# Optimization experiments

Hardware: AMD Instinct MI355X
Metric: run time of the kernel (lower is better)

Reference implementation:

```python
import jax, jax.numpy as jnp
import numpy as np


def _skew(w):
    # standard hat operator: skew(w) @ u = w x u (matches pytorch3d `hat`)
    x, y, z = w[..., 0], w[..., 1], w[..., 2]
    o = jnp.zeros_like(x)
    return jnp.stack([
        jnp.stack([o, -z, y], -1),
        jnp.stack([z, o, -x], -1),
        jnp.stack([-y, x, o], -1),
    ], -2)


def _se3_exp(dof):
    # pytorch3d se3_exp_map convention: dof[..., :3] = translation log, dof[..., 3:] = rotation log.
    # Returns R (column-vector rotation) and T such that p' = R p + T, equivalent to
    # pytorch3d's row-vector matrix M = [[R^T, 0], [T, 1]] used by Rotate/Translate.
    EPS = 1e-4
    v, w = dof[..., :3], dof[..., 3:]
    theta2 = jnp.sum(w * w, axis=-1)
    theta = jnp.sqrt(theta2)
    small = theta < EPS
    safe_t = jnp.where(small, 1.0, theta)
    safe_t2 = jnp.where(small, 1.0, theta2)
    safe_t3 = jnp.where(small, 1.0, theta2 * theta)
    A = jnp.where(small, 1.0 - theta2 / 6.0, jnp.sin(theta) / safe_t)            # sin(t)/t
    B = jnp.where(small, 0.5 - theta2 / 24.0, (1.0 - jnp.cos(theta)) / safe_t2)  # (1-cos t)/t^2
    C = jnp.where(small, 1.0 / 6.0 - theta2 / 120.0,
                  (theta - jnp.sin(theta)) / safe_t3)                            # (t-sin t)/t^3
    K = _skew(w)
    K2 = K @ K
    I = jnp.eye(3, dtype=dof.dtype)
    R = I + A[..., None, None] * K + B[..., None, None] * K2   # Rodrigues
    V = I + B[..., None, None] * K + C[..., None, None] * K2   # SE3 V-matrix
    T = jnp.einsum('...ij,...j->...i', V, v)
    return R, T


def setup_inputs() -> dict:
    key = jax.random.key(0)
    k1, k2 = jax.random.split(key)
    B, NT, NP = 32, 32, 8192  # batch, teeth, points per tooth
    X_v = jax.random.normal(k1, (B, NT, NP, 3), dtype=jnp.float32)
    dof = jax.random.normal(k2, (B, NT, 6), dtype=jnp.float32)
    return {"X_v": X_v, "dof": dof}


def reference(X_v, dof):
    # Fused, fully batched version of the per-(batch, tooth) loop:
    # assembled[:, t] = Rotate(R[:, t]).compose(Translate(T[:, t])).transform_points(X_v[:, t])
    R, T = _se3_exp(dof)                                   # R: [B,NT,3,3], T: [B,NT,3]
    # row-vector convention p @ R_stored + T with R_stored = R^T  ==  R p + T
    return jnp.einsum('btij,btnj->btni', R, X_v) + T[:, :, None, :]
```

## Files before the change

kernel.cpp:

```cpp
#include <hip/hip_runtime.h>


__global__ __launch_bounds__(256) void se3_apply_kernel(
    const float* __restrict__ X,
    const float* __restrict__ dof,
    float* __restrict__ out,
    int bps)
{
    const int bt  = blockIdx.x / bps;
    const int sub = blockIdx.x % bps;

    const float* d = dof + bt * 6;
    const float vx = d[0], vy = d[1], vz = d[2];
    const float wx = d[3], wy = d[4], wz = d[5];

    const float th2 = wx*wx + wy*wy + wz*wz;
    const float th  = sqrtf(th2);
    float A, Bc, C;
    if (th < 1e-4f) {
        A  = 1.0f - th2 * (1.0f/6.0f);
        Bc = 0.5f - th2 * (1.0f/24.0f);
        C  = (1.0f/6.0f) - th2 * (1.0f/120.0f);
    } else {
        const float s = sinf(th);
        const float c = cosf(th);
        A  = s / th;
        Bc = (1.0f - c) / th2;
        C  = (th - s) / (th2 * th);
    }

    const float r00 = 1.0f + Bc*(wx*wx - th2);
    const float r01 = Bc*wx*wy - A*wz;
    const float r02 = Bc*wx*wz + A*wy;
    const float r10 = Bc*wy*wx + A*wz;
    const float r11 = 1.0f + Bc*(wy*wy - th2);
    const float r12 = Bc*wy*wz - A*wx;
    const float r20 = Bc*wz*wx - A*wy;
    const float r21 = Bc*wz*wy + A*wx;
    const float r22 = 1.0f + Bc*(wz*wz - th2);

    const float q00 = 1.0f + C*(wx*wx - th2);
    const float q01 = C*wx*wy - Bc*wz;
    const float q02 = C*wx*wz + Bc*wy;
    const float q10 = C*wy*wx + Bc*wz;
    const float q11 = 1.0f + C*(wy*wy - th2);
    const float q12 = C*wy*wz - Bc*wx;
    const float q20 = C*wz*wx - Bc*wy;
    const float q21 = C*wz*wy + Bc*wx;
    const float q22 = 1.0f + C*(wz*wz - th2);

    const float Tx = q00*vx + q01*vy + q02*vz;
    const float Ty = q10*vx + q11*vy + q12*vz;
    const float Tz = q20*vx + q21*vy + q22*vz;

    const int base = bt * (bps * 256 * 12) + sub * (256 * 12) + (int)threadIdx.x * 12;
    const float4* Xi = reinterpret_cast<const float4*>(X + base);
    float4*       Oi = reinterpret_cast<float4*>(out + base);

    const float4 a = Xi[0];
    const float4 b = Xi[1];
    const float4 c = Xi[2];

    float o[12];
    {
        const float x = a.x, y = a.y, z = a.z;
        o[0] = fmaf(r00,x, fmaf(r01,y, fmaf(r02,z, Tx)));
        o[1] = fmaf(r10,x, fmaf(r11,y, fmaf(r12,z, Ty)));
        o[2] = fmaf(r20,x, fmaf(r21,y, fmaf(r22,z, Tz)));
    }
    {
        const float x = a.w, y = b.x, z = b.y;
        o[3] = fmaf(r00,x, fmaf(r01,y, fmaf(r02,z, Tx)));
        o[4] = fmaf(r10,x, fmaf(r11,y, fmaf(r12,z, Ty)));
        o[5] = fmaf(r20,x, fmaf(r21,y, fmaf(r22,z, Tz)));
    }
    {
        const float x = b.z, y = b.w, z = c.x;
        o[6] = fmaf(r00,x, fmaf(r01,y, fmaf(r02,z, Tx)));
        o[7] = fmaf(r10,x, fmaf(r11,y, fmaf(r12,z, Ty)));
        o[8] = fmaf(r20,x, fmaf(r21,y, fmaf(r22,z, Tz)));
    }
    {
        const float x = c.y, y = c.z, z = c.w;
        o[9]  = fmaf(r00,x, fmaf(r01,y, fmaf(r02,z, Tx)));
        o[10] = fmaf(r10,x, fmaf(r11,y, fmaf(r12,z, Ty)));
        o[11] = fmaf(r20,x, fmaf(r21,y, fmaf(r22,z, Tz)));
    }

    Oi[0] = make_float4(o[0], o[1], o[2],  o[3]);
    Oi[1] = make_float4(o[4], o[5], o[6],  o[7]);
    Oi[2] = make_float4(o[8], o[9], o[10], o[11]);
}

extern "C" void kernel_launch(void* const* d_in, const int* in_sizes, int n_in,
                              void* d_out, int out_size, void* d_ws, size_t ws_size,
                              hipStream_t stream) {
    const float* X   = (const float*)d_in[0];
    const float* dof = (const float*)d_in[1];
    float* out = (float*)d_out;

    const int BT = in_sizes[1] / 6;
    const int NP = in_sizes[0] / (BT * 3);
    const int bps = (NP * 3) / (256 * 12);

    se3_apply_kernel<<<dim3(BT * bps), dim3(256), 0, stream>>>(X, dof, out, bps);
}
```

Measured before the change: 37.53 us.

## Stage point tiles through LDS for coalesced loads and nontemporal stores

Each thread now loads and stores contiguous float4 strides across the block, so every wavefront access is fully coalesced, and uses shared memory to transpose back to per-thread groups of four points. The SE3 exponential is computed once per block by thread 0 and shared through LDS instead of by every thread. Output is written with nontemporal stores to avoid polluting the cache. The cost is two block barriers and extra LDS traffic per element.

```diff
diff --git a/kernel.cpp b/kernel.cpp
--- a/kernel.cpp
+++ b/kernel.cpp
@@ -1,95 +1,118 @@
 #include <hip/hip_runtime.h>
 
 
-__global__ __launch_bounds__(256) void se3_apply_kernel(
-    const float* __restrict__ X,
+typedef float f4 __attribute__((ext_vector_type(4)));
+
+#define TPB 256
+
+__global__ __launch_bounds__(TPB) void se3_apply_kernel(
+    const f4* __restrict__ X4,
     const float* __restrict__ dof,
-    float* __restrict__ out,
+    f4* __restrict__ O4,
     int bps)
 {
+    __shared__ f4 lds4[768];
+    __shared__ float rt[12];
+
     const int bt  = blockIdx.x / bps;
     const int sub = blockIdx.x % bps;
+    const int t   = (int)threadIdx.x;
 
-    const float* d = dof + bt * 6;
-    const float vx = d[0], vy = d[1], vz = d[2];
-    const float wx = d[3], wy = d[4], wz = d[5];
+    const int base4 = (bt * bps + sub) * 768;
 
-    const float th2 = wx*wx + wy*wy + wz*wz;
-    const float th  = sqrtf(th2);
-    float A, Bc, C;
-    if (th < 1e-4f) {
-        A  = 1.0f - th2 * (1.0f/6.0f);
-        Bc = 0.5f - th2 * (1.0f/24.0f);
-        C  = (1.0f/6.0f) - th2 * (1.0f/120.0f);
-    } else {
-        const float s = sinf(th);
-        const float c = cosf(th);
-        A  = s / th;
-        Bc = (1.0f - c) / th2;
-        C  = (th - s) / (th2 * th);
+    const f4 g0 = X4[base4 + t];
+    const f4 g1 = X4[base4 + 256 + t];
+    const f4 g2 = X4[base4 + 512 + t];
+
+    if (t == 0) {
+        const float* d = dof + bt * 6;
+        const float vx = d[0], vy = d[1], vz = d[2];
+        const float wx = d[3], wy = d[4], wz = d[5];
+        const float th2 = wx*wx + wy*wy + wz*wz;
+        const float th  = sqrtf(th2);
+        float A, Bc, C;
+        if (th < 1e-4f) {
+            A  = 1.0f - th2 * (1.0f/6.0f);
+            Bc = 0.5f - th2 * (1.0f/24.0f);
+            C  = (1.0f/6.0f) - th2 * (1.0f/120.0f);
+        } else {
+            const float s = sinf(th);
+            const float c = cosf(th);
+            A  = s / th;
+            Bc = (1.0f - c) / th2;
+            C  = (th - s) / (th2 * th);
+        }
+        rt[0] = 1.0f + Bc*(wx*wx - th2);
+        rt[1] = Bc*wx*wy - A*wz;
+        rt[2] = Bc*wx*wz + A*wy;
+        rt[3] = Bc*wy*wx + A*wz;
+        rt[4] = 1.0f + Bc*(wy*wy - th2);
+        rt[5] = Bc*wy*wz - A*wx;
+        rt[6] = Bc*wz*wx - A*wy;
+        rt[7] = Bc*wz*wy + A*wx;
+        rt[8] = 1.0f + Bc*(wz*wz - th2);
+        const float q00 = 1.0f + C*(wx*wx - th2);
+        const float q01 = C*wx*wy - Bc*wz;
+        const float q02 = C*wx*wz + Bc*wy;
+        const float q10 = C*wy*wx + Bc*wz;
+        const float q11 = 1.0f + C*(wy*wy - th2);
+        const float q12 = C*wy*wz - Bc*wx;
+        const float q20 = C*wz*wx - Bc*wy;
+        const float q21 = C*wz*wy + Bc*wx;
+        const float q22 = 1.0f + C*(wz*wz - th2);
+        rt[9]  = q00*vx + q01*vy + q02*vz;
+        rt[10] = q10*vx + q11*vy + q12*vz;
+        rt[11] = q20*vx + q21*vy + q22*vz;
     }
 
-    const float r00 = 1.0f + Bc*(wx*wx - th2);
-    const float r01 = Bc*wx*wy - A*wz;
-    const float r02 = Bc*wx*wz + A*wy;
-    const float r10 = Bc*wy*wx + A*wz;
-    const float r11 = 1.0f + Bc*(wy*wy - th2);
-    const float r12 = Bc*wy*wz - A*wx;
-    const float r20 = Bc*wz*wx - A*wy;
-    const float r21 = Bc*wz*wy + A*wx;
-    const float r22 = 1.0f + Bc*(wz*wz - th2);
+    lds4[t]       = g0;
+    lds4[t + 256] = g1;
+    lds4[t + 512] = g2;
+    __syncthreads();
 
-    const float q00 = 1.0f + C*(wx*wx - th2);
-    const float q01 = C*wx*wy - Bc*wz;
-    const float q02 = C*wx*wz + Bc*wy;
-    const float q10 = C*wy*wx + Bc*wz;
-    const float q11 = 1.0f + C*(wy*wy - th2);
-    const float q12 = C*wy*wz - Bc*wx;
-    const float q20 = C*wz*wx - Bc*wy;
-    const float q21 = C*wz*wy + Bc*wx;
-    const float q22 = 1.0f + C*(wz*wz - th2);
+    const float r00 = rt[0], r01 = rt[1], r02 = rt[2];
+    const float r10 = rt[3], r11 = rt[4], r12 = rt[5];
+    const float r20 = rt[6], r21 = rt[7], r22 = rt[8];
+    const float Tx  = rt[9], Ty = rt[10], Tz = rt[11];
 
-    const float Tx = q00*vx + q01*vy + q02*vz;
-    const float Ty = q10*vx + q11*vy + q12*vz;
-    const float Tz = q20*vx + q21*vy + q22*vz;
+    const f4 a = lds4[3*t];
+    const f4 b = lds4[3*t + 1];
+    const f4 c = lds4[3*t + 2];
 
-    const int base = bt * (bps * 256 * 12) + sub * (256 * 12) + (int)threadIdx.x * 12;
-    const float4* Xi = reinterpret_cast<const float4*>(X + base);
-    float4*       Oi = reinterpret_cast<float4*>(out + base);
-
-    const float4 a = Xi[0];
-    const float4 b = Xi[1];
-    const float4 c = Xi[2];
-
-    float o[12];
+    f4 oa, ob, oc;
     {
         const float x = a.x, y = a.y, z = a.z;
-        o[0] = fmaf(r00,x, fmaf(r01,y, fmaf(r02,z, Tx)));
-        o[1] = fmaf(r10,x, fmaf(r11,y, fmaf(r12,z, Ty)));
-        o[2] = fmaf(r20,x, fmaf(r21,y, fmaf(r22,z, Tz)));
+        oa.x = fmaf(r00,x, fmaf(r01,y, fmaf(r02,z, Tx)));
+        oa.y = fmaf(r10,x, fmaf(r11,y, fmaf(r12,z, Ty)));
+        oa.z = fmaf(r20,x, fmaf(r21,y, fmaf(r22,z, Tz)));
     }
     {
         const float x = a.w, y = b.x, z = b.y;
-        o[3] = fmaf(r00,x, fmaf(r01,y, fmaf(r02,z, Tx)));
-        o[4] = fmaf(r10,x, fmaf(r11,y, fmaf(r12,z, Ty)));
-        o[5] = fmaf(r20,x, fmaf(r21,y, fmaf(r22,z, Tz)));
+        oa.w = fmaf(r00,x, fmaf(r01,y, fmaf(r02,z, Tx)));
+        ob.x = fmaf(r10,x, fmaf(r11,y, fmaf(r12,z, Ty)));
+        ob.y = fmaf(r20,x, fmaf(r21,y, fmaf(r22,z, Tz)));
     }
     {
         const float x = b.z, y = b.w, z = c.x;
-        o[6] = fmaf(r00,x, fmaf(r01,y, fmaf(r02,z, Tx)));
-        o[7] = fmaf(r10,x, fmaf(r11,y, fmaf(r12,z, Ty)));
-        o[8] = fmaf(r20,x, fmaf(r21,y, fmaf(r22,z, Tz)));
+        ob.z = fmaf(r00,x, fmaf(r01,y, fmaf(r02,z, Tx)));
+        ob.w = fmaf(r10,x, fmaf(r11,y, fmaf(r12,z, Ty)));
+        oc.x = fmaf(r20,x, fmaf(r21,y, fmaf(r22,z, Tz)));
     }
     {
         const float x = c.y, y = c.z, z = c.w;
-        o[9]  = fmaf(r00,x, fmaf(r01,y, fmaf(r02,z, Tx)));
-        o[10] = fmaf(r10,x, fmaf(r11,y, fmaf(r12,z, Ty)));
-        o[11] = fmaf(r20,x, fmaf(r21,y, fmaf(r22,z, Tz)));
+        oc.y = fmaf(r00,x, fmaf(r01,y, fmaf(r02,z, Tx)));
+        oc.z = fmaf(r10,x, fmaf(r11,y, fmaf(r12,z, Ty)));
+        oc.w = fmaf(r20,x, fmaf(r21,y, fmaf(r22,z, Tz)));
     }
 
-    Oi[0] = make_float4(o[0], o[1], o[2],  o[3]);
-    Oi[1] = make_float4(o[4], o[5], o[6],  o[7]);
-    Oi[2] = make_float4(o[8], o[9], o[10], o[11]);
+    lds4[3*t]     = oa;
+    lds4[3*t + 1] = ob;
+    lds4[3*t + 2] = oc;
+    __syncthreads();
+
+    __builtin_nontemporal_store(lds4[t],       &O4[base4 + t]);
+    __builtin_nontemporal_store(lds4[t + 256], &O4[base4 + 256 + t]);
+    __builtin_nontemporal_store(lds4[t + 512], &O4[base4 + 512 + t]);
 }
 
 extern "C" void kernel_launch(void* const* d_in, const int* in_sizes, int n_in,
@@ -101,7 +124,8 @@
 
     const int BT = in_sizes[1] / 6;
     const int NP = in_sizes[0] / (BT * 3);
-    const int bps = (NP * 3) / (256 * 12);
+    const int bps = NP / 1024;
 
-    se3_apply_kernel<<<dim3(BT * bps), dim3(256), 0, stream>>>(X, dof, out, bps);
+    se3_apply_kernel<<<dim3(BT * bps), dim3(TPB), 0, stream>>>(
+        (const f4*)X, dof, (f4*)out, bps);
 }
```

New measurement: 34.40 us. 1.09x faster.
